# Optimization experiments

Hardware: AMD Instinct MI355X
Metric: run time of the kernel (lower is better)

## Reference

```python
import jax, jax.numpy as jnp
import numpy as np

E = 800000   # num edges
N = 50000    # num atoms
C = 128      # in_channels
RBF = 20     # rbf_dim
T = 1        # num_target


def setup_inputs() -> dict:
    key = jax.random.key(0)
    ks = jax.random.split(key, 12)
    return {
        "x_scalar": jax.random.normal(ks[0], (E, C), dtype=jnp.float32),
        "rbf": jax.random.normal(ks[1], (E, RBF), dtype=jnp.float32),
        "envelop_para": jax.random.uniform(ks[2], (E, 1), dtype=jnp.float32),
        "edge_index_0": jax.random.randint(ks[3], (E,), 0, N),
        "num_atoms": N,
        # learned parameters (biases initialized to zero per reset_parameters)
        "W_rbf": jax.random.normal(ks[4], (C, RBF), dtype=jnp.float32) * 0.05,
        "b_rbf": jnp.zeros((C,), dtype=jnp.float32),
        "W1": jax.random.normal(ks[5], (C, C), dtype=jnp.float32) * 0.05,
        "b1": jnp.zeros((C,), dtype=jnp.float32),
        "W2": jax.random.normal(ks[6], (C, C), dtype=jnp.float32) * 0.05,
        "b2": jnp.zeros((C,), dtype=jnp.float32),
        "W3": jax.random.normal(ks[7], (T, C), dtype=jnp.float32) * 0.05,
        "b3": jnp.zeros((T,), dtype=jnp.float32),
    }


def reference(x_scalar, rbf, envelop_para, edge_index_0, num_atoms,
              W_rbf, b_rbf, W1, b1, W2, b2, W3, b3):
    # per-edge filter: Linear(rbf) * envelope, then modulate node features
    rbf_filter = (rbf @ W_rbf.T + b_rbf) * envelop_para  # [E, C]
    msg = rbf_filter * x_scalar                           # [E, C]
    # scatter_add over destination atoms
    out = jax.ops.segment_sum(msg, edge_index_0, num_segments=num_atoms)  # [N, C]
    # small MLP head: Linear+SiLU, Linear+SiLU, Linear -> num_target
    out = jax.nn.silu(out @ W1.T + b1)
    out = jax.nn.silu(out @ W2.T + b2)
    out = out @ W3.T + b3                                 # [N, T]
    return out
```

## Files before the change

kernel.cpp:

```cpp
#include <hip/hip_runtime.h>
#include <hip/hip_bf16.h>

#define C 128
#define RBFD 20
#define NATOMS 50000
#define SCAN_CHUNK 1024
#define SLAB 128
#define SS 32
#define NSS (SLAB / SS)

__global__ __launch_bounds__(256) void setup_kernel(
    const float* __restrict__ W1, const float* __restrict__ W2,
    float* __restrict__ W1T, float* __restrict__ W2T,
    int* __restrict__ count, float4* __restrict__ acc4,
    int n, int acc_quads)
{
    const int t = blockIdx.x * blockDim.x + threadIdx.x;
    const int stride = gridDim.x * blockDim.x;
    if (t < C * C) {
        int k = t / C;
        int c = t % C;
        W1T[t] = W1[c * C + k];
        W2T[t] = W2[c * C + k];
    }
    for (int i = t; i < n; i += stride) count[i] = 0;
    const float4 z = make_float4(0.f, 0.f, 0.f, 0.f);
    for (int i = t; i < acc_quads; i += stride) acc4[i] = z;
}

__global__ __launch_bounds__(256) void histogram_kernel(
    const int* __restrict__ idx, int* __restrict__ count, int E)
{
    int e = blockIdx.x * blockDim.x + threadIdx.x;
    if (e < E) atomicAdd(&count[idx[e]], 1);
}

__global__ __launch_bounds__(256) void scan_partials_kernel(
    const int* __restrict__ count, int* __restrict__ partial, int n)
{
    __shared__ int sm[256];
    const int start = blockIdx.x * SCAN_CHUNK;
    int s = 0;
    for (int i = threadIdx.x; i < SCAN_CHUNK; i += 256) {
        int g = start + i;
        if (g < n) s += count[g];
    }
    sm[threadIdx.x] = s;
    __syncthreads();
    for (int off = 128; off > 0; off >>= 1) {
        if (threadIdx.x < off) sm[threadIdx.x] += sm[threadIdx.x + off];
        __syncthreads();
    }
    if (threadIdx.x == 0) partial[blockIdx.x] = sm[0];
}

__global__ void scan_chunkbase_kernel(int* __restrict__ partial,
                                      int* __restrict__ base,
                                      int nchunks, int n)
{
    if (threadIdx.x == 0 && blockIdx.x == 0) {
        int run = 0;
        for (int k = 0; k < nchunks; ++k) {
            int t = partial[k];
            partial[k] = run;
            run += t;
        }
        base[n] = run;
    }
}

__global__ __launch_bounds__(1024) void scan_apply_kernel(
    const int* __restrict__ count, const int* __restrict__ chunk_base,
    int* __restrict__ base, int* __restrict__ cursor, int n)
{
    __shared__ int sm[SCAN_CHUNK];
    const int t = threadIdx.x;
    const int i = blockIdx.x * SCAN_CHUNK + t;
    int v = (i < n) ? count[i] : 0;
    sm[t] = v;
    __syncthreads();
    for (int off = 1; off < SCAN_CHUNK; off <<= 1) {
        int tmp = (t >= off) ? sm[t - off] : 0;
        __syncthreads();
        sm[t] += tmp;
        __syncthreads();
    }
    if (i < n) {
        int excl = sm[t] - v + chunk_base[blockIdx.x];
        base[i] = excl;
        cursor[i] = excl;
    }
}

__global__ __launch_bounds__(256) void fill_perm_kernel(
    const int* __restrict__ idx, int* __restrict__ cursor,
    int* __restrict__ perm, int* __restrict__ own, int E)
{
    int e = blockIdx.x * blockDim.x + threadIdx.x;
    if (e < E) {
        int a = idx[e];
        int pos = atomicAdd(&cursor[a], 1);
        perm[pos] = e;
        own[pos] = a;
    }
}

__global__ __launch_bounds__(128, 2) void gather_kernel(
    const float* __restrict__ x,
    const float* __restrict__ rbf,
    const float* __restrict__ env,
    const int*   __restrict__ perm,
    const int*   __restrict__ own,
    const float* __restrict__ Wrbf,
    const float* __restrict__ brbf,
    float* __restrict__ acc)
{
    __shared__ int   e_s[SLAB];
    __shared__ float env_s[SLAB];
    __shared__ int   own_s[SLAB];
    __shared__ float rbf_s[2][SS][RBFD];

    const int tid = threadIdx.x;
    const int p0  = blockIdx.x * SLAB;

    {
        const int e = perm[p0 + tid];
        e_s[tid]   = e;
        env_s[tid] = env[e];
        own_s[tid] = own[p0 + tid];
    }

    float w[RBFD];
#pragma unroll
    for (int r = 0; r < RBFD; ++r) w[r] = Wrbf[tid * RBFD + r];
    const float bias = brbf[tid];

    __syncthreads();

    const int first_own = own_s[0];
    int   cur_own = first_own;
    float sum = 0.0f;

#define FLUSH()                                                                \
    do {                                                                       \
        if (cur_own == first_own)                                              \
            unsafeAtomicAdd(&acc[(size_t)cur_own * C + tid], sum);             \
        else acc[(size_t)cur_own * C + tid] = sum;                             \
    } while (0)

    float xr[2][SS];
    float st[5];

#pragma unroll
    for (int p = 0; p < 5; ++p) {
        const int g = p * 128 + tid;
        st[p] = rbf[(size_t)e_s[g / RBFD] * RBFD + (g % RBFD)];
    }
#pragma unroll
    for (int i = 0; i < SS; ++i)
        xr[0][i] = x[(size_t)e_s[i] * C + tid];
    __builtin_amdgcn_sched_barrier(0);
#pragma unroll
    for (int p = 0; p < 5; ++p) {
        const int g = p * 128 + tid;
        rbf_s[0][g / RBFD][g % RBFD] = st[p];
    }
    __syncthreads();

#pragma unroll
    for (int ss = 0; ss < NSS; ++ss) {
        const int sbase = ss * SS;
        const int cur   = ss & 1;

        if (ss + 1 < NSS) {
#pragma unroll
            for (int p = 0; p < 5; ++p) {
                const int g = p * 128 + tid;
                st[p] = rbf[(size_t)e_s[sbase + SS + g / RBFD] * RBFD + (g % RBFD)];
            }
#pragma unroll
            for (int i = 0; i < SS; ++i)
                xr[cur ^ 1][i] = x[(size_t)e_s[sbase + SS + i] * C + tid];
        }
        __builtin_amdgcn_sched_barrier(0);

#pragma unroll
        for (int j = 0; j < SS; ++j) {
            const float4* q = reinterpret_cast<const float4*>(&rbf_s[cur][j][0]);
            const float4 a = q[0], b = q[1], c = q[2], d = q[3], e4 = q[4];
            float f = bias;
            f = fmaf(a.x,  w[0],  f); f = fmaf(a.y,  w[1],  f);
            f = fmaf(a.z,  w[2],  f); f = fmaf(a.w,  w[3],  f);
            f = fmaf(b.x,  w[4],  f); f = fmaf(b.y,  w[5],  f);
            f = fmaf(b.z,  w[6],  f); f = fmaf(b.w,  w[7],  f);
            f = fmaf(c.x,  w[8],  f); f = fmaf(c.y,  w[9],  f);
            f = fmaf(c.z,  w[10], f); f = fmaf(c.w,  w[11], f);
            f = fmaf(d.x,  w[12], f); f = fmaf(d.y,  w[13], f);
            f = fmaf(d.z,  w[14], f); f = fmaf(d.w,  w[15], f);
            f = fmaf(e4.x, w[16], f); f = fmaf(e4.y, w[17], f);
            f = fmaf(e4.z, w[18], f); f = fmaf(e4.w, w[19], f);

            const float v = f * env_s[sbase + j] * xr[cur][j];
            const int   o = own_s[sbase + j];
            if (o != cur_own) { FLUSH(); sum = 0.0f; cur_own = o; }
            sum += v;
        }
        __builtin_amdgcn_sched_barrier(0);

        if (ss + 1 < NSS) {
#pragma unroll
            for (int p = 0; p < 5; ++p) {
                const int g = p * 128 + tid;
                rbf_s[cur ^ 1][g / RBFD][g % RBFD] = st[p];
            }
            asm volatile("s_waitcnt lgkmcnt(0)" ::: "memory");
            __builtin_amdgcn_sched_barrier(0);
            __builtin_amdgcn_s_barrier();
        }
    }
    unsafeAtomicAdd(&acc[(size_t)cur_own * C + tid], sum);
#undef FLUSH
}

__device__ __forceinline__ float silu_f(float v) {
    return v * (1.0f / (1.0f + __expf(-v)));
}

__global__ __launch_bounds__(256) void mlp_head_kernel(
    const float* __restrict__ acc,
    const float* __restrict__ W1T,
    const float* __restrict__ b1,
    const float* __restrict__ W2T,
    const float* __restrict__ b2,
    const float* __restrict__ W3,
    const float* __restrict__ b3,
    float* __restrict__ out,
    int natoms)
{
    __shared__ float As[C][C + 1];

    const int tid = threadIdx.x;
    const int a0  = blockIdx.x * C;
    const int tc  = tid & 15;
    const int ta  = tid >> 4;
    const int abase = ta * 8;
    const int cbase = tc * 8;

    {
        const int sub = tid >> 7;
        const int k   = tid & 127;
        for (int pair = 0; pair < 64; ++pair) {
            const int al = pair * 2 + sub;
            const int a  = a0 + al;
            float v = (a < natoms) ? acc[(size_t)a * C + k] : 0.0f;
            As[k][al] = v;
        }
    }
    __syncthreads();

    float r[8][8];

#pragma unroll
    for (int i = 0; i < 8; ++i)
#pragma unroll
        for (int j = 0; j < 8; ++j) r[i][j] = 0.0f;

#pragma unroll 2
    for (int k = 0; k < C; ++k) {
        float4 bq0 = *reinterpret_cast<const float4*>(W1T + k * C + cbase);
        float4 bq1 = *reinterpret_cast<const float4*>(W1T + k * C + cbase + 4);
        float bv[8] = {bq0.x, bq0.y, bq0.z, bq0.w, bq1.x, bq1.y, bq1.z, bq1.w};
        float av[8];
#pragma unroll
        for (int i = 0; i < 8; ++i) av[i] = As[k][abase + i];
#pragma unroll
        for (int i = 0; i < 8; ++i)
#pragma unroll
            for (int j = 0; j < 8; ++j) r[i][j] = fmaf(av[i], bv[j], r[i][j]);
    }

    __syncthreads();
    {
        float bb[8];
#pragma unroll
        for (int j = 0; j < 8; ++j) bb[j] = b1[cbase + j];
#pragma unroll
        for (int i = 0; i < 8; ++i)
#pragma unroll
            for (int j = 0; j < 8; ++j)
                As[cbase + j][abase + i] = silu_f(r[i][j] + bb[j]);
    }
    __syncthreads();

#pragma unroll
    for (int i = 0; i < 8; ++i)
#pragma unroll
        for (int j = 0; j < 8; ++j) r[i][j] = 0.0f;

#pragma unroll 2
    for (int k = 0; k < C; ++k) {
        float4 bq0 = *reinterpret_cast<const float4*>(W2T + k * C + cbase);
        float4 bq1 = *reinterpret_cast<const float4*>(W2T + k * C + cbase + 4);
        float bv[8] = {bq0.x, bq0.y, bq0.z, bq0.w, bq1.x, bq1.y, bq1.z, bq1.w};
        float av[8];
#pragma unroll
        for (int i = 0; i < 8; ++i) av[i] = As[k][abase + i];
#pragma unroll
        for (int i = 0; i < 8; ++i)
#pragma unroll
            for (int j = 0; j < 8; ++j) r[i][j] = fmaf(av[i], bv[j], r[i][j]);
    }

    __syncthreads();

    {
        float bb[8], w3v[8];
#pragma unroll
        for (int j = 0; j < 8; ++j) bb[j] = b2[cbase + j];
        float4 wq0 = *reinterpret_cast<const float4*>(W3 + cbase);
        float4 wq1 = *reinterpret_cast<const float4*>(W3 + cbase + 4);
        w3v[0]=wq0.x; w3v[1]=wq0.y; w3v[2]=wq0.z; w3v[3]=wq0.w;
        w3v[4]=wq1.x; w3v[5]=wq1.y; w3v[6]=wq1.z; w3v[7]=wq1.w;

#pragma unroll
        for (int i = 0; i < 8; ++i) {
            float p = 0.0f;
#pragma unroll
            for (int j = 0; j < 8; ++j)
                p = fmaf(silu_f(r[i][j] + bb[j]), w3v[j], p);
            As[abase + i][tc] = p;
        }
    }
    __syncthreads();

    if (tid < C) {
        const int a = a0 + tid;
        if (a < natoms) {
            float s = 0.0f;
#pragma unroll
            for (int t = 0; t < 16; ++t) s += As[tid][t];
            out[a] = s + b3[0];
        }
    }
}

extern "C" void kernel_launch(void* const* d_in, const int* in_sizes, int n_in,
                              void* d_out, int out_size, void* d_ws, size_t ws_size,
                              hipStream_t stream) {
    const float* x      = (const float*)d_in[0];
    const float* rbf    = (const float*)d_in[1];
    const float* env    = (const float*)d_in[2];
    const int*   idx    = (const int*)  d_in[3];
    const float* Wrbf   = (const float*)d_in[5];
    const float* brbf   = (const float*)d_in[6];
    const float* W1     = (const float*)d_in[7];
    const float* b1     = (const float*)d_in[8];
    const float* W2     = (const float*)d_in[9];
    const float* b2     = (const float*)d_in[10];
    const float* W3     = (const float*)d_in[11];
    const float* b3     = (const float*)d_in[12];
    float*       out    = (float*)d_out;

    const int E = in_sizes[0] / C;
    const int N = NATOMS;
    const int nchunks = (N + SCAN_CHUNK - 1) / SCAN_CHUNK;

    float* acc     = (float*)d_ws;
    float* W1T     = acc + (size_t)N * C;
    float* W2T     = W1T + C * C;
    int*   count   = (int*)(W2T + C * C);
    int*   base    = count + N;
    int*   cursor  = base + (N + 1);
    int*   partial = cursor + N;
    int*   perm    = partial + 64;
    int*   own     = perm + E;

    setup_kernel<<<2048, 256, 0, stream>>>(W1, W2, W1T, W2T, count,
                                           (float4*)acc, N, (N * C) / 4);

    histogram_kernel<<<(E + 255) / 256, 256, 0, stream>>>(idx, count, E);
    scan_partials_kernel<<<nchunks, 256, 0, stream>>>(count, partial, N);
    scan_chunkbase_kernel<<<1, 64, 0, stream>>>(partial, base, nchunks, N);
    scan_apply_kernel<<<nchunks, SCAN_CHUNK, 0, stream>>>(count, partial, base, cursor, N);
    fill_perm_kernel<<<(E + 255) / 256, 256, 0, stream>>>(idx, cursor, perm, own, E);

    gather_kernel<<<E / SLAB, 128, 0, stream>>>(x, rbf, env, perm, own,
                                                Wrbf, brbf, acc);

    const int tiles = (N + C - 1) / C;
    mlp_head_kernel<<<tiles, 256, 0, stream>>>(acc, W1T, b1, W2T, b2, W3, b3, out, N);
}
```

Measured before the change: 331.1 us.

## Merge scan into single-block kernel and make gather kernel persistent

Replaces the three-kernel chunked prefix scan over atom counts with one single-block kernel in which each thread scans a contiguous run of counts serially before a block-level scan. This removes two kernel launches and the serial single-thread chunk-base pass. The gather kernel becomes grid-stride over slabs with a fixed 2048 blocks, so Wrbf weights are loaded once per block rather than once per slab. The trade-offs are fewer in-flight blocks for latency hiding in the gather, and each slab boundary now needs its own atomic flush.

```diff
diff --git a/kernel.cpp b/kernel.cpp
--- a/kernel.cpp
+++ b/kernel.cpp
@@ -4,7 +4,6 @@
 #define C 128
 #define RBFD 20
 #define NATOMS 50000
-#define SCAN_CHUNK 1024
 #define SLAB 128
 #define SS 32
 #define NSS (SLAB / SS)
@@ -35,61 +34,47 @@
     if (e < E) atomicAdd(&count[idx[e]], 1);
 }
 
-__global__ __launch_bounds__(256) void scan_partials_kernel(
-    const int* __restrict__ count, int* __restrict__ partial, int n)
-{
-    __shared__ int sm[256];
-    const int start = blockIdx.x * SCAN_CHUNK;
-    int s = 0;
-    for (int i = threadIdx.x; i < SCAN_CHUNK; i += 256) {
-        int g = start + i;
-        if (g < n) s += count[g];
-    }
-    sm[threadIdx.x] = s;
-    __syncthreads();
-    for (int off = 128; off > 0; off >>= 1) {
-        if (threadIdx.x < off) sm[threadIdx.x] += sm[threadIdx.x + off];
-        __syncthreads();
-    }
-    if (threadIdx.x == 0) partial[blockIdx.x] = sm[0];
-}
-
-__global__ void scan_chunkbase_kernel(int* __restrict__ partial,
-                                      int* __restrict__ base,
-                                      int nchunks, int n)
-{
-    if (threadIdx.x == 0 && blockIdx.x == 0) {
-        int run = 0;
-        for (int k = 0; k < nchunks; ++k) {
-            int t = partial[k];
-            partial[k] = run;
-            run += t;
-        }
-        base[n] = run;
-    }
-}
-
-__global__ __launch_bounds__(1024) void scan_apply_kernel(
-    const int* __restrict__ count, const int* __restrict__ chunk_base,
-    int* __restrict__ base, int* __restrict__ cursor, int n)
-{
-    __shared__ int sm[SCAN_CHUNK];
-    const int t = threadIdx.x;
-    const int i = blockIdx.x * SCAN_CHUNK + t;
-    int v = (i < n) ? count[i] : 0;
-    sm[t] = v;
-    __syncthreads();
-    for (int off = 1; off < SCAN_CHUNK; off <<= 1) {
+#define SCAN_T 1024
+#define SCAN_CH ((NATOMS + SCAN_T - 1) / SCAN_T)
+
+__global__ __launch_bounds__(SCAN_T) void scan_kernel(
+    const int* __restrict__ count, int* __restrict__ base,
+    int* __restrict__ cursor)
+{
+    __shared__ int sm[SCAN_T];
+    const int t  = threadIdx.x;
+    const int s0 = t * SCAN_CH;
+
+    int v[SCAN_CH];
+#pragma unroll
+    for (int k = 0; k < SCAN_CH; ++k) {
+        const int i = s0 + k;
+        v[k] = (i < NATOMS) ? count[i] : 0;
+    }
+    int run = 0;
+#pragma unroll
+    for (int k = 0; k < SCAN_CH; ++k) { int tv = v[k]; v[k] = run; run += tv; }
+
+    sm[t] = run;
+    __syncthreads();
+    for (int off = 1; off < SCAN_T; off <<= 1) {
         int tmp = (t >= off) ? sm[t - off] : 0;
         __syncthreads();
         sm[t] += tmp;
         __syncthreads();
     }
-    if (i < n) {
-        int excl = sm[t] - v + chunk_base[blockIdx.x];
-        base[i] = excl;
-        cursor[i] = excl;
-    }
+    const int offset = sm[t] - run;
+
+#pragma unroll
+    for (int k = 0; k < SCAN_CH; ++k) {
+        const int i = s0 + k;
+        if (i < NATOMS) {
+            const int b = v[k] + offset;
+            base[i]   = b;
+            cursor[i] = b;
+        }
+    }
+    if (t == SCAN_T - 1) base[NATOMS] = sm[SCAN_T - 1];
 }
 
 __global__ __launch_bounds__(256) void fill_perm_kernel(
@@ -113,7 +98,8 @@
     const int*   __restrict__ own,
     const float* __restrict__ Wrbf,
     const float* __restrict__ brbf,
-    float* __restrict__ acc)
+    float* __restrict__ acc,
+    int nslabs)
 {
     __shared__ int   e_s[SLAB];
     __shared__ float env_s[SLAB];
@@ -121,25 +107,11 @@
     __shared__ float rbf_s[2][SS][RBFD];
 
     const int tid = threadIdx.x;
-    const int p0  = blockIdx.x * SLAB;
-
-    {
-        const int e = perm[p0 + tid];
-        e_s[tid]   = e;
-        env_s[tid] = env[e];
-        own_s[tid] = own[p0 + tid];
-    }
 
     float w[RBFD];
 #pragma unroll
     for (int r = 0; r < RBFD; ++r) w[r] = Wrbf[tid * RBFD + r];
     const float bias = brbf[tid];
-
-    __syncthreads();
-
-    const int first_own = own_s[0];
-    int   cur_own = first_own;
-    float sum = 0.0f;
 
 #define FLUSH()                                                                \
     do {                                                                       \
@@ -148,77 +120,94 @@
         else acc[(size_t)cur_own * C + tid] = sum;                             \
     } while (0)
 
-    float xr[2][SS];
-    float st[5];
-
-#pragma unroll
-    for (int p = 0; p < 5; ++p) {
-        const int g = p * 128 + tid;
-        st[p] = rbf[(size_t)e_s[g / RBFD] * RBFD + (g % RBFD)];
-    }
-#pragma unroll
-    for (int i = 0; i < SS; ++i)
-        xr[0][i] = x[(size_t)e_s[i] * C + tid];
-    __builtin_amdgcn_sched_barrier(0);
-#pragma unroll
-    for (int p = 0; p < 5; ++p) {
-        const int g = p * 128 + tid;
-        rbf_s[0][g / RBFD][g % RBFD] = st[p];
-    }
-    __syncthreads();
-
-#pragma unroll
-    for (int ss = 0; ss < NSS; ++ss) {
-        const int sbase = ss * SS;
-        const int cur   = ss & 1;
-
-        if (ss + 1 < NSS) {
-#pragma unroll
-            for (int p = 0; p < 5; ++p) {
-                const int g = p * 128 + tid;
-                st[p] = rbf[(size_t)e_s[sbase + SS + g / RBFD] * RBFD + (g % RBFD)];
+    for (int slab = blockIdx.x; slab < nslabs; slab += gridDim.x) {
+        const int p0 = slab * SLAB;
+
+        __syncthreads();
+        {
+            const int e = perm[p0 + tid];
+            e_s[tid]   = e;
+            env_s[tid] = env[e];
+            own_s[tid] = own[p0 + tid];
+        }
+        __syncthreads();
+
+        const int first_own = own_s[0];
+        int   cur_own = first_own;
+        float sum = 0.0f;
+
+        float xr[2][SS];
+        float st[5];
+
+#pragma unroll
+        for (int p = 0; p < 5; ++p) {
+            const int g = p * 128 + tid;
+            st[p] = rbf[(size_t)e_s[g / RBFD] * RBFD + (g % RBFD)];
+        }
+#pragma unroll
+        for (int i = 0; i < SS; ++i)
+            xr[0][i] = x[(size_t)e_s[i] * C + tid];
+        __builtin_amdgcn_sched_barrier(0);
+#pragma unroll
+        for (int p = 0; p < 5; ++p) {
+            const int g = p * 128 + tid;
+            rbf_s[0][g / RBFD][g % RBFD] = st[p];
+        }
+        __syncthreads();
+
+#pragma unroll
+        for (int ss = 0; ss < NSS; ++ss) {
+            const int sbase = ss * SS;
+            const int cur   = ss & 1;
+
+            if (ss + 1 < NSS) {
+#pragma unroll
+                for (int p = 0; p < 5; ++p) {
+                    const int g = p * 128 + tid;
+                    st[p] = rbf[(size_t)e_s[sbase + SS + g / RBFD] * RBFD + (g % RBFD)];
+                }
+#pragma unroll
+                for (int i = 0; i < SS; ++i)
+                    xr[cur ^ 1][i] = x[(size_t)e_s[sbase + SS + i] * C + tid];
             }
-#pragma unroll
-            for (int i = 0; i < SS; ++i)
-                xr[cur ^ 1][i] = x[(size_t)e_s[sbase + SS + i] * C + tid];
-        }
-        __builtin_amdgcn_sched_barrier(0);
-
-#pragma unroll
-        for (int j = 0; j < SS; ++j) {
-            const float4* q = reinterpret_cast<const float4*>(&rbf_s[cur][j][0]);
-            const float4 a = q[0], b = q[1], c = q[2], d = q[3], e4 = q[4];
-            float f = bias;
-            f = fmaf(a.x,  w[0],  f); f = fmaf(a.y,  w[1],  f);
-            f = fmaf(a.z,  w[2],  f); f = fmaf(a.w,  w[3],  f);
-            f = fmaf(b.x,  w[4],  f); f = fmaf(b.y,  w[5],  f);
-            f = fmaf(b.z,  w[6],  f); f = fmaf(b.w,  w[7],  f);
-            f = fmaf(c.x,  w[8],  f); f = fmaf(c.y,  w[9],  f);
-            f = fmaf(c.z,  w[10], f); f = fmaf(c.w,  w[11], f);
-            f = fmaf(d.x,  w[12], f); f = fmaf(d.y,  w[13], f);
-            f = fmaf(d.z,  w[14], f); f = fmaf(d.w,  w[15], f);
-            f = fmaf(e4.x, w[16], f); f = fmaf(e4.y, w[17], f);
-            f = fmaf(e4.z, w[18], f); f = fmaf(e4.w, w[19], f);
-
-            const float v = f * env_s[sbase + j] * xr[cur][j];
-            const int   o = own_s[sbase + j];
-            if (o != cur_own) { FLUSH(); sum = 0.0f; cur_own = o; }
-            sum += v;
-        }
-        __builtin_amdgcn_sched_barrier(0);
-
-        if (ss + 1 < NSS) {
-#pragma unroll
-            for (int p = 0; p < 5; ++p) {
-                const int g = p * 128 + tid;
-                rbf_s[cur ^ 1][g / RBFD][g % RBFD] = st[p];
+            __builtin_amdgcn_sched_barrier(0);
+
+#pragma unroll
+            for (int j = 0; j < SS; ++j) {
+                const float4* q = reinterpret_cast<const float4*>(&rbf_s[cur][j][0]);
+                const float4 a = q[0], b = q[1], c = q[2], d = q[3], e4 = q[4];
+                float f = bias;
+                f = fmaf(a.x,  w[0],  f); f = fmaf(a.y,  w[1],  f);
+                f = fmaf(a.z,  w[2],  f); f = fmaf(a.w,  w[3],  f);
+                f = fmaf(b.x,  w[4],  f); f = fmaf(b.y,  w[5],  f);
+                f = fmaf(b.z,  w[6],  f); f = fmaf(b.w,  w[7],  f);
+                f = fmaf(c.x,  w[8],  f); f = fmaf(c.y,  w[9],  f);
+                f = fmaf(c.z,  w[10], f); f = fmaf(c.w,  w[11], f);
+                f = fmaf(d.x,  w[12], f); f = fmaf(d.y,  w[13], f);
+                f = fmaf(d.z,  w[14], f); f = fmaf(d.w,  w[15], f);
+                f = fmaf(e4.x, w[16], f); f = fmaf(e4.y, w[17], f);
+                f = fmaf(e4.z, w[18], f); f = fmaf(e4.w, w[19], f);
+
+                const float v = f * env_s[sbase + j] * xr[cur][j];
+                const int   o = own_s[sbase + j];
+                if (o != cur_own) { FLUSH(); sum = 0.0f; cur_own = o; }
+                sum += v;
             }
-            asm volatile("s_waitcnt lgkmcnt(0)" ::: "memory");
             __builtin_amdgcn_sched_barrier(0);
-            __builtin_amdgcn_s_barrier();
-        }
-    }
-    unsafeAtomicAdd(&acc[(size_t)cur_own * C + tid], sum);
+
+            if (ss + 1 < NSS) {
+#pragma unroll
+                for (int p = 0; p < 5; ++p) {
+                    const int g = p * 128 + tid;
+                    rbf_s[cur ^ 1][g / RBFD][g % RBFD] = st[p];
+                }
+                asm volatile("s_waitcnt lgkmcnt(0)" ::: "memory");
+                __builtin_amdgcn_sched_barrier(0);
+                __builtin_amdgcn_s_barrier();
+            }
+        }
+        unsafeAtomicAdd(&acc[(size_t)cur_own * C + tid], sum);
+    }
 #undef FLUSH
 }
 
@@ -363,7 +352,6 @@
 
     const int E = in_sizes[0] / C;
     const int N = NATOMS;
-    const int nchunks = (N + SCAN_CHUNK - 1) / SCAN_CHUNK;
 
     float* acc     = (float*)d_ws;
     float* W1T     = acc + (size_t)N * C;
@@ -371,21 +359,18 @@
     int*   count   = (int*)(W2T + C * C);
     int*   base    = count + N;
     int*   cursor  = base + (N + 1);
-    int*   partial = cursor + N;
-    int*   perm    = partial + 64;
+    int*   perm    = cursor + N;
     int*   own     = perm + E;
 
     setup_kernel<<<2048, 256, 0, stream>>>(W1, W2, W1T, W2T, count,
                                            (float4*)acc, N, (N * C) / 4);
 
     histogram_kernel<<<(E + 255) / 256, 256, 0, stream>>>(idx, count, E);
-    scan_partials_kernel<<<nchunks, 256, 0, stream>>>(count, partial, N);
-    scan_chunkbase_kernel<<<1, 64, 0, stream>>>(partial, base, nchunks, N);
-    scan_apply_kernel<<<nchunks, SCAN_CHUNK, 0, stream>>>(count, partial, base, cursor, N);
+    scan_kernel<<<1, SCAN_T, 0, stream>>>(count, base, cursor);
     fill_perm_kernel<<<(E + 255) / 256, 256, 0, stream>>>(idx, cursor, perm, own, E);
 
-    gather_kernel<<<E / SLAB, 128, 0, stream>>>(x, rbf, env, perm, own,
-                                                Wrbf, brbf, acc);
+    gather_kernel<<<2048, 128, 0, stream>>>(x, rbf, env, perm, own,
+                                            Wrbf, brbf, acc, E / SLAB);
 
     const int tiles = (N + C - 1) / C;
     mlp_head_kernel<<<tiles, 256, 0, stream>>>(acc, W1T, b1, W2T, b2, W3, b3, out, N);
```

After: 443.3 us. 33.9% more time.
